# Kernel tuning notes

Measured on AMD Instinct MI355X. Metric: run time of the kernel, lower is better.

The kernel has to match this reference:

```python
import jax, jax.numpy as jnp
import numpy as np

B_, K_, D_, L_, N_, R_ = 4, 4, 96, 2048, 16, 6
C_ = R_ + 2 * N_  # 38


def setup_inputs() -> dict:
    key = jax.random.key(0)
    ks = jax.random.split(key, 6)
    scale = 0.05  # keep projections in a realistic range (like 1/sqrt(fan_in) init)
    return {
        "xs": jax.random.normal(ks[0], (B_, K_, D_, L_), dtype=jnp.float32),
        "A_logs": jax.random.uniform(ks[1], (K_ * D_, N_), dtype=jnp.float32),
        "Ds": jax.random.normal(ks[2], (K_ * D_,), dtype=jnp.float32),
        "dt_projs_weight": jax.random.normal(ks[3], (K_, D_, R_), dtype=jnp.float32) * scale,
        "dt_projs_bias": jax.random.normal(ks[4], (K_, D_), dtype=jnp.float32) * scale,
        "x_proj_weight": jax.random.normal(ks[5], (K_, C_, D_), dtype=jnp.float32) * scale,
    }


def reference(xs, A_logs, Ds, dt_projs_weight, dt_projs_bias, x_proj_weight):
    B, K, D, L = xs.shape
    N = A_logs.shape[1]
    R = dt_projs_weight.shape[2]

    xs = xs.astype(jnp.float32)  # force_fp32=True

    # project x -> (delta, B, C):  [B,K,C,L]
    x_dbl = jnp.einsum("bkdl,kcd->bkcl", xs, x_proj_weight)
    dts, Bs, Cs = x_dbl[:, :, :R], x_dbl[:, :, R:R + N], x_dbl[:, :, R + N:]
    # dt low-rank -> per-channel delta: [B,K,D,L]
    dts = jnp.einsum("bkrl,kdr->bkdl", dts, dt_projs_weight)

    A = -jnp.exp(A_logs.astype(jnp.float32)).reshape(K, D, N)  # [K,D,N]
    Dskd = Ds.astype(jnp.float32).reshape(K, D)

    # delta_softplus with delta_bias
    delta = jax.nn.softplus(dts + dt_projs_bias.astype(jnp.float32)[None, :, :, None])

    # discretization: deltaA [B,K,D,L,N], deltaB_u [B,K,D,L,N]
    dA = jnp.exp(delta[..., None] * A[None, :, :, None, :])
    dBu = jnp.einsum("bkdl,bknl,bkdl->bkdln", delta, Bs, xs)

    # linear recurrence h_t = dA_t * h_{t-1} + dBu_t via parallel associative scan over L
    def combine(e1, e2):
        a1, b1 = e1
        a2, b2 = e2
        return a1 * a2, a2 * b1 + b2

    _, hs = jax.lax.associative_scan(combine, (dA, dBu), axis=3)  # hs: [B,K,D,L,N]

    # y_t = C_t . h_t + D * x_t
    y = jnp.einsum("bkdln,bknl->bkdl", hs, Cs) + Dskd[None, :, :, None] * xs
    return y.astype(jnp.float32)  # [B,K,D,L]
```

## Files before the change

kernel.cpp:

```cpp
#include <hip/hip_runtime.h>
#include <hip/hip_fp16.h>
#include <math.h>

#define B_ 4
#define K_ 4
#define D_ 96
#define L_ 2048
#define N_ 16
#define R_ 6
#define C_ 38
#define CH 16
#define TPR 128

__device__ __forceinline__ float softplus_f(float x) {
    return fmaxf(x, 0.f) + __logf(1.f + __expf(-fabsf(x)));
}

#if __has_builtin(__builtin_amdgcn_exp2f)
__device__ __forceinline__ float exp2_fast(float x) { return __builtin_amdgcn_exp2f(x); }
#else
__device__ __forceinline__ float exp2_fast(float x) { return __expf(0.6931471805599453f * x); }
#endif

__device__ __forceinline__ float h2f(const uint4& v, int e) {
    return __half2float(((const __half*)&v)[e]);
}


__global__ __launch_bounds__(256) void proj_kernel(
    const float* __restrict__ xs, const float* __restrict__ xpw,
    uint4* __restrict__ BCc, float* __restrict__ dts_ws)
{
    __shared__ float sWt[D_][8];
    const int bk = blockIdx.x;
    const int k = bk & 3;
    const int cg = blockIdx.z;
    const int tid = threadIdx.x;

    int c0, nr;
    if (cg < 4)       { c0 = R_ + cg * 8; nr = 8; }
    else if (cg == 4) { c0 = 0;           nr = 4; }
    else              { c0 = 4;           nr = 2; }

    for (int i = tid; i < 8 * D_; i += 256) {
        const int r = i / D_, dd = i % D_;
        sWt[dd][r] = (r < nr) ? xpw[(k * C_ + c0 + r) * D_ + dd] : 0.f;
    }
    __syncthreads();

    const int l = blockIdx.y * 256 + tid;
    const float* Xl = xs + (size_t)bk * D_ * L_ + l;

    float acc[8];
#pragma unroll
    for (int r = 0; r < 8; ++r) acc[r] = 0.f;

#pragma unroll
    for (int d = 0; d < D_; ++d) {
        const float xv = Xl[d * L_];
        float4 w0 = *(const float4*)&sWt[d][0];
        float4 w1 = *(const float4*)&sWt[d][4];
        acc[0] = fmaf(w0.x, xv, acc[0]); acc[1] = fmaf(w0.y, xv, acc[1]);
        acc[2] = fmaf(w0.z, xv, acc[2]); acc[3] = fmaf(w0.w, xv, acc[3]);
        acc[4] = fmaf(w1.x, xv, acc[4]); acc[5] = fmaf(w1.y, xv, acc[5]);
        acc[6] = fmaf(w1.z, xv, acc[6]); acc[7] = fmaf(w1.w, xv, acc[7]);
    }

    if (cg < 4) {
        const int i8 = l & 15, t8 = l >> 4;
        union { __half h[8]; uint4 v; } p;
#pragma unroll
        for (int e = 0; e < 8; ++e) p.h[e] = __float2half(acc[e]);
        BCc[(((size_t)bk * 16 + i8) * 4 + cg) * TPR + t8] = p.v;
    } else {
        const int rbase = (cg == 4) ? 0 : 4;
        const int rcnt = (cg == 4) ? 4 : 2;
        for (int r = 0; r < rcnt; ++r)
            dts_ws[((size_t)bk * R_ + rbase + r) * L_ + l] = acc[r];
    }
}

__global__ __launch_bounds__(256) void scan_kernel(
    const float* __restrict__ xs, const float* __restrict__ A_logs,
    const float* __restrict__ Ds, const float* __restrict__ dtw,
    const float* __restrict__ dtb, const float* __restrict__ dts_ws,
    const uint4* __restrict__ BCc, float* __restrict__ out)
{
    __shared__ float sAw[4][8];
    __shared__ float sBw[4][8];
    __shared__ float sy[TPR][17];

    const int bkd = blockIdx.x;
    const int d = bkd % D_;
    const int bk = bkd / D_;
    const int k = bk & 3;
    const int kd = k * D_ + d;
    const int tid = threadIdx.x;
    const int g = tid >> 7;
    const int t = tid & (TPR - 1);
    const int lane = tid & 63;
    const int gw = tid >> 6;

    const uint4* BC = BCc + (size_t)bk * 16 * 4 * TPR;
    const int jB = g, jC = 2 + g;

    const float4* xv4 = (const float4*)(xs + (size_t)bkd * L_);
    float x[CH];
#pragma unroll
    for (int q = 0; q < 4; ++q)
        *(float4*)&x[q * 4] = xv4[t * 4 + q];

    float del[CH];
    const float bias = dtb[kd];
#pragma unroll
    for (int j = 0; j < CH; ++j) del[j] = bias;
    const float* w2 = dtw + (size_t)kd * R_;
    const float4* dts4 = (const float4*)(dts_ws + (size_t)bk * R_ * L_);
#pragma unroll
    for (int r = 0; r < R_; ++r) {
        const float wr = w2[r];
#pragma unroll
        for (int q = 0; q < 4; ++q) {
            const float4 tv = dts4[r * (L_ / 4) + t * 4 + q];
            del[q * 4 + 0] = fmaf(wr, tv.x, del[q * 4 + 0]);
            del[q * 4 + 1] = fmaf(wr, tv.y, del[q * 4 + 1]);
            del[q * 4 + 2] = fmaf(wr, tv.z, del[q * 4 + 2]);
            del[q * 4 + 3] = fmaf(wr, tv.w, del[q * 4 + 3]);
        }
    }
#pragma unroll
    for (int j = 0; j < CH; ++j) del[j] = softplus_f(del[j]);

    float A2[8];
    const float* Ap = A_logs + (size_t)kd * N_ + g * 8;
#pragma unroll
    for (int n = 0; n < 8; ++n) A2[n] = -__expf(Ap[n]) * 1.44269504f;
    const float Dval = Ds[kd];

    float a[8], b[8];
#pragma unroll
    for (int n = 0; n < 8; ++n) { a[n] = 1.f; b[n] = 0.f; }
#pragma unroll
    for (int i = 0; i < CH; ++i) {
        const uint4 cB = BC[(i * 4 + jB) * TPR + t];
        const float dl = del[i];
        const float dx = dl * x[i];
#pragma unroll
        for (int n = 0; n < 8; ++n) {
            const float dA = exp2_fast(dl * A2[n]);
            b[n] = fmaf(dA, b[n], dx * h2f(cB, n));
            a[n] *= dA;
        }
    }

#pragma unroll
    for (int off = 1; off < 64; off <<= 1) {
#pragma unroll
        for (int n = 0; n < 8; ++n) {
            const float pa = __shfl_up(a[n], off, 64);
            const float pb = __shfl_up(b[n], off, 64);
            if (lane >= off) {
                b[n] = fmaf(a[n], pb, b[n]);
                a[n] *= pa;
            }
        }
    }
    if (lane == 63) {
#pragma unroll
        for (int n = 0; n < 8; ++n) { sAw[gw][n] = a[n]; sBw[gw][n] = b[n]; }
    }
    __syncthreads();

    float h[8];
#pragma unroll
    for (int n = 0; n < 8; ++n) {
        float ae = __shfl_up(a[n], 1, 64);
        float be = __shfl_up(b[n], 1, 64);
        if (lane == 0) { ae = 1.f; be = 0.f; }
        float wb = 0.f;
        for (int w = g * 2; w < gw; ++w) wb = fmaf(sAw[w][n], wb, sBw[w][n]);
        h[n] = fmaf(ae, wb, be);
    }

    float yv[CH];
#pragma unroll
    for (int i = 0; i < CH; ++i) {
        const uint4 cB = BC[(i * 4 + jB) * TPR + t];
        const uint4 cC = BC[(i * 4 + jC) * TPR + t];
        const float dl = del[i];
        const float dx = dl * x[i];
        float y = (g == 0) ? Dval * x[i] : 0.f;
#pragma unroll
        for (int n = 0; n < 8; ++n) {
            const float dA = exp2_fast(dl * A2[n]);
            h[n] = fmaf(dA, h[n], dx * h2f(cB, n));
            y = fmaf(h[n], h2f(cC, n), y);
        }
        yv[i] = y;
    }

    if (g == 1) {
#pragma unroll
        for (int j = 0; j < CH; ++j) sy[t][j] = yv[j];
    }
    __syncthreads();
    if (g == 0) {
#pragma unroll
        for (int j = 0; j < CH; ++j) yv[j] += sy[t][j];
        float4* ov = (float4*)(out + (size_t)bkd * L_);
#pragma unroll
        for (int q = 0; q < 4; ++q)
            ov[t * 4 + q] = make_float4(yv[q * 4], yv[q * 4 + 1],
                                        yv[q * 4 + 2], yv[q * 4 + 3]);
    }
}

extern "C" void kernel_launch(void* const* d_in, const int* in_sizes, int n_in,
                              void* d_out, int out_size, void* d_ws, size_t ws_size,
                              hipStream_t stream) {
    const float* xs = (const float*)d_in[0];
    const float* A_logs = (const float*)d_in[1];
    const float* Ds = (const float*)d_in[2];
    const float* dtw = (const float*)d_in[3];
    const float* dtb = (const float*)d_in[4];
    const float* xpw = (const float*)d_in[5];
    float* out = (float*)d_out;

    uint4* BCc = (uint4*)d_ws;
    float* dts_ws = (float*)(BCc + (size_t)B_ * K_ * 16 * 4 * TPR);

    proj_kernel<<<dim3(B_ * K_, 8, 6), 256, 0, stream>>>(xs, xpw, BCc, dts_ws);
    scan_kernel<<<B_ * K_ * D_, 256, 0, stream>>>(
        xs, A_logs, Ds, dtw, dtb, dts_ws, BCc, out);
}
```

Measured before the change: 113.3 us.

## Merge state halves into one thread and widen projection per block

```diff
diff --git a/kernel.cpp b/kernel.cpp
--- a/kernel.cpp
+++ b/kernel.cpp
@@ -31,78 +31,81 @@
     const float* __restrict__ xs, const float* __restrict__ xpw,
     uint4* __restrict__ BCc, float* __restrict__ dts_ws)
 {
-    __shared__ float sWt[D_][8];
+    __shared__ float sWt[D_][24];
     const int bk = blockIdx.x;
     const int k = bk & 3;
     const int cg = blockIdx.z;
     const int tid = threadIdx.x;
 
-    int c0, nr;
-    if (cg < 4)       { c0 = R_ + cg * 8; nr = 8; }
-    else if (cg == 4) { c0 = 0;           nr = 4; }
-    else              { c0 = 4;           nr = 2; }
-
-    for (int i = tid; i < 8 * D_; i += 256) {
-        const int r = i / D_, dd = i % D_;
-        sWt[dd][r] = (r < nr) ? xpw[(k * C_ + c0 + r) * D_ + dd] : 0.f;
+    for (int idx = tid; idx < 24 * D_; idx += 256) {
+        const int m = idx / D_, dd = idx % D_;
+        float wv = 0.f;
+        if (cg == 0) {
+            if (m < 16)      wv = xpw[(k * C_ + R_ + m) * D_ + dd];
+            else if (m < 22) wv = xpw[(k * C_ + (m - 16)) * D_ + dd];
+        } else {
+            if (m < 16)      wv = xpw[(k * C_ + R_ + 16 + m) * D_ + dd];
+        }
+        sWt[dd][m] = wv;
     }
     __syncthreads();
 
     const int l = blockIdx.y * 256 + tid;
     const float* Xl = xs + (size_t)bk * D_ * L_ + l;
 
-    float acc[8];
-#pragma unroll
-    for (int r = 0; r < 8; ++r) acc[r] = 0.f;
+    float acc[24];
+#pragma unroll
+    for (int m = 0; m < 24; ++m) acc[m] = 0.f;
 
 #pragma unroll
     for (int d = 0; d < D_; ++d) {
         const float xv = Xl[d * L_];
-        float4 w0 = *(const float4*)&sWt[d][0];
-        float4 w1 = *(const float4*)&sWt[d][4];
-        acc[0] = fmaf(w0.x, xv, acc[0]); acc[1] = fmaf(w0.y, xv, acc[1]);
-        acc[2] = fmaf(w0.z, xv, acc[2]); acc[3] = fmaf(w0.w, xv, acc[3]);
-        acc[4] = fmaf(w1.x, xv, acc[4]); acc[5] = fmaf(w1.y, xv, acc[5]);
-        acc[6] = fmaf(w1.z, xv, acc[6]); acc[7] = fmaf(w1.w, xv, acc[7]);
-    }
-
-    if (cg < 4) {
-        const int i8 = l & 15, t8 = l >> 4;
-        union { __half h[8]; uint4 v; } p;
-#pragma unroll
-        for (int e = 0; e < 8; ++e) p.h[e] = __float2half(acc[e]);
-        BCc[(((size_t)bk * 16 + i8) * 4 + cg) * TPR + t8] = p.v;
-    } else {
-        const int rbase = (cg == 4) ? 0 : 4;
-        const int rcnt = (cg == 4) ? 4 : 2;
-        for (int r = 0; r < rcnt; ++r)
-            dts_ws[((size_t)bk * R_ + rbase + r) * L_ + l] = acc[r];
-    }
-}
-
-__global__ __launch_bounds__(256) void scan_kernel(
+#pragma unroll
+        for (int q = 0; q < 6; ++q) {
+            const float4 w = *(const float4*)&sWt[d][q * 4];
+            acc[q * 4 + 0] = fmaf(w.x, xv, acc[q * 4 + 0]);
+            acc[q * 4 + 1] = fmaf(w.y, xv, acc[q * 4 + 1]);
+            acc[q * 4 + 2] = fmaf(w.z, xv, acc[q * 4 + 2]);
+            acc[q * 4 + 3] = fmaf(w.w, xv, acc[q * 4 + 3]);
+        }
+    }
+
+    const int i8 = l & 15, t8 = l >> 4;
+    const int jb = cg * 2;
+    union { __half h[8]; uint4 v; } p0, p1;
+#pragma unroll
+    for (int e = 0; e < 8; ++e) {
+        p0.h[e] = __float2half(acc[e]);
+        p1.h[e] = __float2half(acc[8 + e]);
+    }
+    BCc[(((size_t)bk * 16 + i8) * 4 + jb) * TPR + t8] = p0.v;
+    BCc[(((size_t)bk * 16 + i8) * 4 + jb + 1) * TPR + t8] = p1.v;
+
+    if (cg == 0) {
+#pragma unroll
+        for (int r = 0; r < R_; ++r)
+            dts_ws[((size_t)bk * R_ + r) * L_ + l] = acc[16 + r];
+    }
+}
+
+__global__ __launch_bounds__(128) void scan_kernel(
     const float* __restrict__ xs, const float* __restrict__ A_logs,
     const float* __restrict__ Ds, const float* __restrict__ dtw,
     const float* __restrict__ dtb, const float* __restrict__ dts_ws,
     const uint4* __restrict__ BCc, float* __restrict__ out)
 {
-    __shared__ float sAw[4][8];
-    __shared__ float sBw[4][8];
-    __shared__ float sy[TPR][17];
+    __shared__ float sBw[16];
 
     const int bkd = blockIdx.x;
     const int d = bkd % D_;
     const int bk = bkd / D_;
     const int k = bk & 3;
     const int kd = k * D_ + d;
-    const int tid = threadIdx.x;
-    const int g = tid >> 7;
-    const int t = tid & (TPR - 1);
-    const int lane = tid & 63;
-    const int gw = tid >> 6;
+    const int t = threadIdx.x;
+    const int lane = t & 63;
+    const int w = t >> 6;
 
     const uint4* BC = BCc + (size_t)bk * 16 * 4 * TPR;
-    const int jB = g, jC = 2 + g;
 
     const float4* xv4 = (const float4*)(xs + (size_t)bkd * L_);
     float x[CH];
@@ -131,32 +134,36 @@
 #pragma unroll
     for (int j = 0; j < CH; ++j) del[j] = softplus_f(del[j]);
 
-    float A2[8];
-    const float* Ap = A_logs + (size_t)kd * N_ + g * 8;
-#pragma unroll
-    for (int n = 0; n < 8; ++n) A2[n] = -__expf(Ap[n]) * 1.44269504f;
+    float A2[16];
+    const float* Ap = A_logs + (size_t)kd * N_;
+#pragma unroll
+    for (int n = 0; n < 16; ++n) A2[n] = -__expf(Ap[n]) * 1.44269504f;
     const float Dval = Ds[kd];
 
-    float a[8], b[8];
-#pragma unroll
-    for (int n = 0; n < 8; ++n) { a[n] = 1.f; b[n] = 0.f; }
+    float a[16], b[16];
+#pragma unroll
+    for (int n = 0; n < 16; ++n) { a[n] = 1.f; b[n] = 0.f; }
 #pragma unroll
     for (int i = 0; i < CH; ++i) {
-        const uint4 cB = BC[(i * 4 + jB) * TPR + t];
+        const uint4 cB0 = BC[(i * 4 + 0) * TPR + t];
+        const uint4 cB1 = BC[(i * 4 + 1) * TPR + t];
         const float dl = del[i];
         const float dx = dl * x[i];
 #pragma unroll
         for (int n = 0; n < 8; ++n) {
-            const float dA = exp2_fast(dl * A2[n]);
-            b[n] = fmaf(dA, b[n], dx * h2f(cB, n));
-            a[n] *= dA;
+            const float dA0 = exp2_fast(dl * A2[n]);
+            b[n] = fmaf(dA0, b[n], dx * h2f(cB0, n));
+            a[n] *= dA0;
+            const float dA1 = exp2_fast(dl * A2[8 + n]);
+            b[8 + n] = fmaf(dA1, b[8 + n], dx * h2f(cB1, n));
+            a[8 + n] *= dA1;
         }
     }
 
 #pragma unroll
     for (int off = 1; off < 64; off <<= 1) {
 #pragma unroll
-        for (int n = 0; n < 8; ++n) {
+        for (int n = 0; n < 16; ++n) {
             const float pa = __shfl_up(a[n], off, 64);
             const float pb = __shfl_up(b[n], off, 64);
             if (lane >= off) {
@@ -165,54 +172,49 @@
             }
         }
     }
-    if (lane == 63) {
-#pragma unroll
-        for (int n = 0; n < 8; ++n) { sAw[gw][n] = a[n]; sBw[gw][n] = b[n]; }
+    if (t == 63) {
+#pragma unroll
+        for (int n = 0; n < 16; ++n) sBw[n] = b[n];
     }
     __syncthreads();
 
-    float h[8];
-#pragma unroll
-    for (int n = 0; n < 8; ++n) {
+    float h[16];
+#pragma unroll
+    for (int n = 0; n < 16; ++n) {
         float ae = __shfl_up(a[n], 1, 64);
         float be = __shfl_up(b[n], 1, 64);
         if (lane == 0) { ae = 1.f; be = 0.f; }
-        float wb = 0.f;
-        for (int w = g * 2; w < gw; ++w) wb = fmaf(sAw[w][n], wb, sBw[w][n]);
+        const float wb = w ? sBw[n] : 0.f;
         h[n] = fmaf(ae, wb, be);
     }
 
     float yv[CH];
 #pragma unroll
     for (int i = 0; i < CH; ++i) {
-        const uint4 cB = BC[(i * 4 + jB) * TPR + t];
-        const uint4 cC = BC[(i * 4 + jC) * TPR + t];
+        const uint4 cB0 = BC[(i * 4 + 0) * TPR + t];
+        const uint4 cB1 = BC[(i * 4 + 1) * TPR + t];
+        const uint4 cC0 = BC[(i * 4 + 2) * TPR + t];
+        const uint4 cC1 = BC[(i * 4 + 3) * TPR + t];
         const float dl = del[i];
         const float dx = dl * x[i];
-        float y = (g == 0) ? Dval * x[i] : 0.f;
+        float y = Dval * x[i];
 #pragma unroll
         for (int n = 0; n < 8; ++n) {
-            const float dA = exp2_fast(dl * A2[n]);
-            h[n] = fmaf(dA, h[n], dx * h2f(cB, n));
-            y = fmaf(h[n], h2f(cC, n), y);
+            const float dA0 = exp2_fast(dl * A2[n]);
+            h[n] = fmaf(dA0, h[n], dx * h2f(cB0, n));
+            y = fmaf(h[n], h2f(cC0, n), y);
+            const float dA1 = exp2_fast(dl * A2[8 + n]);
+            h[8 + n] = fmaf(dA1, h[8 + n], dx * h2f(cB1, n));
+            y = fmaf(h[8 + n], h2f(cC1, n), y);
         }
         yv[i] = y;
     }
 
-    if (g == 1) {
-#pragma unroll
-        for (int j = 0; j < CH; ++j) sy[t][j] = yv[j];
-    }
-    __syncthreads();
-    if (g == 0) {
-#pragma unroll
-        for (int j = 0; j < CH; ++j) yv[j] += sy[t][j];
-        float4* ov = (float4*)(out + (size_t)bkd * L_);
-#pragma unroll
-        for (int q = 0; q < 4; ++q)
-            ov[t * 4 + q] = make_float4(yv[q * 4], yv[q * 4 + 1],
-                                        yv[q * 4 + 2], yv[q * 4 + 3]);
-    }
+    float4* ov = (float4*)(out + (size_t)bkd * L_);
+#pragma unroll
+    for (int q = 0; q < 4; ++q)
+        ov[t * 4 + q] = make_float4(yv[q * 4], yv[q * 4 + 1],
+                                    yv[q * 4 + 2], yv[q * 4 + 3]);
 }
 
 extern "C" void kernel_launch(void* const* d_in, const int* in_sizes, int n_in,
@@ -229,7 +231,7 @@
     uint4* BCc = (uint4*)d_ws;
     float* dts_ws = (float*)(BCc + (size_t)B_ * K_ * 16 * 4 * TPR);
 
-    proj_kernel<<<dim3(B_ * K_, 8, 6), 256, 0, stream>>>(xs, xpw, BCc, dts_ws);
-    scan_kernel<<<B_ * K_ * D_, 256, 0, stream>>>(
+    proj_kernel<<<dim3(B_ * K_, 8, 2), 256, 0, stream>>>(xs, xpw, BCc, dts_ws);
+    scan_kernel<<<B_ * K_ * D_, TPR, 0, stream>>>(
         xs, A_logs, Ds, dtw, dtb, dts_ws, BCc, out);
 }
```

New measurement: 135.7 us. 1.2x slower.

## Restructure projection kernel: wider channel tiles with split-D reduction via LDS

Applied to the files above, without the earlier changes.

```diff
diff --git a/kernel.cpp b/kernel.cpp
--- a/kernel.cpp
+++ b/kernel.cpp
@@ -31,52 +31,75 @@
     const float* __restrict__ xs, const float* __restrict__ xpw,
     uint4* __restrict__ BCc, float* __restrict__ dts_ws)
 {
-    __shared__ float sWt[D_][8];
+    __shared__ float sWt[D_][24];
+    __shared__ float sRed[3][64][25];
     const int bk = blockIdx.x;
     const int k = bk & 3;
     const int cg = blockIdx.z;
     const int tid = threadIdx.x;
-
-    int c0, nr;
-    if (cg < 4)       { c0 = R_ + cg * 8; nr = 8; }
-    else if (cg == 4) { c0 = 0;           nr = 4; }
-    else              { c0 = 4;           nr = 2; }
-
-    for (int i = tid; i < 8 * D_; i += 256) {
-        const int r = i / D_, dd = i % D_;
-        sWt[dd][r] = (r < nr) ? xpw[(k * C_ + c0 + r) * D_ + dd] : 0.f;
-    }
-    __syncthreads();
-
-    const int l = blockIdx.y * 256 + tid;
+    const int dg = tid >> 6;
+    const int li = tid & 63;
+
+    for (int idx = tid; idx < 24 * D_; idx += 256) {
+        const int m = idx / D_, dd = idx % D_;
+        float wv = 0.f;
+        if (cg == 0) {
+            if (m < 16)      wv = xpw[(k * C_ + R_ + m) * D_ + dd];
+            else if (m < 22) wv = xpw[(k * C_ + (m - 16)) * D_ + dd];
+        } else {
+            if (m < 16)      wv = xpw[(k * C_ + R_ + 16 + m) * D_ + dd];
+        }
+        sWt[dd][m] = wv;
+    }
+    __syncthreads();
+
+    const int l = blockIdx.y * 64 + li;
     const float* Xl = xs + (size_t)bk * D_ * L_ + l;
 
-    float acc[8];
-#pragma unroll
-    for (int r = 0; r < 8; ++r) acc[r] = 0.f;
-
-#pragma unroll
-    for (int d = 0; d < D_; ++d) {
-        const float xv = Xl[d * L_];
-        float4 w0 = *(const float4*)&sWt[d][0];
-        float4 w1 = *(const float4*)&sWt[d][4];
-        acc[0] = fmaf(w0.x, xv, acc[0]); acc[1] = fmaf(w0.y, xv, acc[1]);
-        acc[2] = fmaf(w0.z, xv, acc[2]); acc[3] = fmaf(w0.w, xv, acc[3]);
-        acc[4] = fmaf(w1.x, xv, acc[4]); acc[5] = fmaf(w1.y, xv, acc[5]);
-        acc[6] = fmaf(w1.z, xv, acc[6]); acc[7] = fmaf(w1.w, xv, acc[7]);
-    }
-
-    if (cg < 4) {
+    float acc[24];
+#pragma unroll
+    for (int m = 0; m < 24; ++m) acc[m] = 0.f;
+
+#pragma unroll
+    for (int dd = 0; dd < 24; ++dd) {
+        const int d = dg * 24 + dd;
+        const float xv = Xl[(size_t)d * L_];
+#pragma unroll
+        for (int q = 0; q < 6; ++q) {
+            const float4 w = *(const float4*)&sWt[d][q * 4];
+            acc[q * 4 + 0] = fmaf(w.x, xv, acc[q * 4 + 0]);
+            acc[q * 4 + 1] = fmaf(w.y, xv, acc[q * 4 + 1]);
+            acc[q * 4 + 2] = fmaf(w.z, xv, acc[q * 4 + 2]);
+            acc[q * 4 + 3] = fmaf(w.w, xv, acc[q * 4 + 3]);
+        }
+    }
+
+    if (dg > 0) {
+#pragma unroll
+        for (int m = 0; m < 24; ++m) sRed[dg - 1][li][m] = acc[m];
+    }
+    __syncthreads();
+    if (dg == 0) {
+#pragma unroll
+        for (int m = 0; m < 24; ++m)
+            acc[m] += sRed[0][li][m] + sRed[1][li][m] + sRed[2][li][m];
+
         const int i8 = l & 15, t8 = l >> 4;
-        union { __half h[8]; uint4 v; } p;
-#pragma unroll
-        for (int e = 0; e < 8; ++e) p.h[e] = __float2half(acc[e]);
-        BCc[(((size_t)bk * 16 + i8) * 4 + cg) * TPR + t8] = p.v;
-    } else {
-        const int rbase = (cg == 4) ? 0 : 4;
-        const int rcnt = (cg == 4) ? 4 : 2;
-        for (int r = 0; r < rcnt; ++r)
-            dts_ws[((size_t)bk * R_ + rbase + r) * L_ + l] = acc[r];
+        const int jb = cg * 2;
+        union { __half h[8]; uint4 v; } p0, p1;
+#pragma unroll
+        for (int e = 0; e < 8; ++e) {
+            p0.h[e] = __float2half(acc[e]);
+            p1.h[e] = __float2half(acc[8 + e]);
+        }
+        BCc[(((size_t)bk * 16 + i8) * 4 + jb) * TPR + t8] = p0.v;
+        BCc[(((size_t)bk * 16 + i8) * 4 + jb + 1) * TPR + t8] = p1.v;
+
+        if (cg == 0) {
+#pragma unroll
+            for (int r = 0; r < R_; ++r)
+                dts_ws[((size_t)bk * R_ + r) * L_ + l] = acc[16 + r];
+        }
     }
 }
 
@@ -229,7 +252,7 @@
     uint4* BCc = (uint4*)d_ws;
     float* dts_ws = (float*)(BCc + (size_t)B_ * K_ * 16 * 4 * TPR);
 
-    proj_kernel<<<dim3(B_ * K_, 8, 6), 256, 0, stream>>>(xs, xpw, BCc, dts_ws);
+    proj_kernel<<<dim3(B_ * K_, 32, 2), 256, 0, stream>>>(xs, xpw, BCc, dts_ws);
     scan_kernel<<<B_ * K_ * D_, 256, 0, stream>>>(
         xs, A_logs, Ds, dtw, dtb, dts_ws, BCc, out);
 }
```

Result: no change. 114.8 us (+1.3%).
